# Performance work log

Measured on AMD Instinct MI355X. Metric: run time of the kernel, lower is better.

## Reference

```python
import jax, jax.numpy as jnp
import numpy as np

POINT_NB = 256
DILATION = 1
EPS = 1e-4  # pad mask value used by shiftFeat (0.0001)


def _shift(where, f, d):
    """Replicate-pad shift of f:[B,C,H,W]; returns shifted features and
    channel-averaged validity mask [B,1,H,W] (1 inside, EPS in pad region)."""
    B, C, H, W = f.shape
    m = jnp.ones((B, 1, H, W), dtype=f.dtype)
    if where == 'none':
        return f, m
    if where == 'left':
        fs = jnp.concatenate([f[..., d:], jnp.broadcast_to(f[..., -1:], (B, C, H, d))], axis=-1)
        m = m.at[..., -d:].set(EPS)
    elif where == 'right':
        fs = jnp.concatenate([jnp.broadcast_to(f[..., :1], (B, C, H, d)), f[..., :-d]], axis=-1)
        m = m.at[..., :d].set(EPS)
    elif where == 'top':
        fs = jnp.concatenate([f[:, :, d:, :], jnp.broadcast_to(f[:, :, -1:, :], (B, C, d, W))], axis=2)
        m = m.at[:, :, -d:, :].set(EPS)
    elif where == 'bot':
        fs = jnp.concatenate([jnp.broadcast_to(f[:, :, :1, :], (B, C, d, W)), f[:, :, :-d, :]], axis=2)
        m = m.at[:, :, :d, :].set(EPS)
    else:
        raise ValueError(where)
    return fs, m


def _cos_sim(f1, f2, m1, m2):
    # sim = sum(f1*f2*m1*m2, C) / (||m1*f1|| * ||m2*f2||); masks are [B,1,H,W], m>0
    num = (m1 * m2) * jnp.sum(f1 * f2, axis=1, keepdims=True)
    den = (m1 * jnp.sqrt(jnp.sum(f1 * f1, axis=1, keepdims=True))) * \
          (m2 * jnp.sqrt(jnp.sum(f2 * f2, axis=1, keepdims=True)))
    return num / den


def _total_sim(features, d):
    f1, m1 = _shift('right', features, d)
    f2, m2 = _shift('left', features, d)
    horiz = _cos_sim(f1, f2, m1, m2)
    f1, m1 = _shift('top', features, d)
    f2, m2 = _shift('bot', features, d)
    verti = _cos_sim(f1, f2, m1, m2)
    return (horiz + verti) * 0.5  # [B,1,H,W]


def setup_inputs() -> dict:
    key = jax.random.key(0)
    features = jax.random.normal(key, (16, 256, 56, 56), dtype=jnp.float32)
    return {"features": features}


def reference(features):
    B, C, H, W = features.shape
    sim = _total_sim(features, DILATION)            # [B,1,H,W]
    flat = sim.reshape(B, H * W)                    # [B,HW]
    vals, idx = jax.lax.top_k(flat, POINT_NB)       # [B,K]
    ycoord = idx // W
    xcoord = idx % W
    # gather feature vectors at selected points: [B,C,HW] -> [B,K,C]
    feat_flat = features.reshape(B, C, H * W)
    point_feat = jnp.take_along_axis(feat_flat, idx[:, None, :], axis=2)
    point_feat = jnp.transpose(point_feat, (0, 2, 1))
    return point_feat, vals, ycoord, xcoord
```

## Files before the change

kernel.cpp:

```cpp
#include <hip/hip_runtime.h>

#define NB 16
#define NC 256
#define NH 56
#define NW 56
#define NHW (NH * NW)
#define NK 256
#define CAP 1024

#define BR 8
#define RS 10
#define CS 8
#define CQ 64
#define NCHUNK (CQ / CS)
#define CHUNK16 (CS * RS * NW / 4)
#define NBAND (NH / BR)
#define P1_BLOCKS (NB * NBAND * 4)
#define NQ (BR * (NW / 4))
#define MAPS (NB * NHW)

#define GPX 112
#define GNT (NHW / GPX)
#define GCC 64
#define GCH16 (GCC * GPX * 4 / 16)

__device__ inline unsigned int flip_f32(float f) {
    unsigned int u = __float_as_uint(f);
    return (u & 0x80000000u) ? ~u : (u | 0x80000000u);
}
__device__ inline float unflip_f32(unsigned int u) {
    u = (u & 0x80000000u) ? (u ^ 0x80000000u) : ~u;
    return __uint_as_float(u);
}

__global__ void __launch_bounds__(256)
pass1_kernel(const float* __restrict__ f, float* __restrict__ maps) {
    __shared__ __align__(16) float buf[2][CS * RS * NW];
    __shared__ float redbuf[NQ][2][12];

    int bid = blockIdx.x;
    int sb = (bid & 7) * (P1_BLOCKS / 8) + (bid >> 3);
    int b = sb / 28;
    int rem0 = sb - b * 28;
    int band = rem0 >> 2;
    int chq = rem0 & 3;
    int y0 = band * BR;
    int tid = threadIdx.x;
    const float* fb = f + (size_t)b * NC * NHW + (size_t)chq * CQ * NHW;

    auto stage = [&](int ci, float* dst) {
        int c0 = ci * CS;
#pragma unroll
        for (int i = 0; i < 5; ++i) {
            int k = tid + 256 * i;
            if (k < CHUNK16) {
                int ch = k / (RS * 14);
                int rem = k - ch * (RS * 14);
                int rl = rem / 14;
                int xk = rem - rl * 14;
                int rg = y0 - 1 + rl;
                rg = rg < 0 ? 0 : (rg > NH - 1 ? NH - 1 : rg);
                const float* src = fb + (size_t)(c0 + ch) * NHW + rg * NW + xk * 4;
                __builtin_amdgcn_global_load_lds(
                    (const __attribute__((address_space(1))) void*)src,
                    (__attribute__((address_space(3))) void*)(dst + k * 4),
                    16, 0, 0);
            }
        }
    };

    int chg = tid / NQ;
    int quad = tid - chg * NQ;
    int r = quad / 14, qx = quad - r * 14, x0 = qx * 4;
    int xl = x0 ? x0 - 1 : 0;
    int xr = (x0 + 4 < NW) ? x0 + 4 : NW - 1;

    float n0 = 0.f, n1 = 0.f, n2 = 0.f, n3 = 0.f;
    float h0 = 0.f, h1 = 0.f, h2 = 0.f, h3 = 0.f;
    float w0 = 0.f, w1 = 0.f, w2 = 0.f, w3 = 0.f;

    stage(0, buf[0]);
    __syncthreads();
    for (int ci = 0; ci < NCHUNK; ++ci) {
        if (ci + 1 < NCHUNK) stage(ci + 1, buf[(ci + 1) & 1]);
        if (tid < 2 * NQ) {
            const float* sbf = buf[ci & 1];
#pragma unroll
            for (int c = 0; c < 4; ++c) {
                const float* Bm = sbf + (chg * 4 + c) * (RS * NW) + (r + 1) * NW;
                float4 v = *(const float4*)(Bm + x0);
                float  l = Bm[xl];
                float  rr = Bm[xr];
                float4 u = *(const float4*)(Bm + NW + x0);
                float4 d = *(const float4*)(Bm - NW + x0);
                n0 += v.x * v.x; n1 += v.y * v.y; n2 += v.z * v.z; n3 += v.w * v.w;
                h0 += l * v.y;   h1 += v.x * v.z; h2 += v.y * v.w; h3 += v.z * rr;
                w0 += u.x * d.x; w1 += u.y * d.y; w2 += u.z * d.z; w3 += u.w * d.w;
            }
        }
        __syncthreads();
    }

    if (tid < 2 * NQ) {
        float* rb = redbuf[quad][chg];
        rb[0] = n0; rb[1] = n1; rb[2]  = n2; rb[3]  = n3;
        rb[4] = h0; rb[5] = h1; rb[6]  = h2; rb[7]  = h3;
        rb[8] = w0; rb[9] = w1; rb[10] = w2; rb[11] = w3;
    }
    __syncthreads();

    float* mbase = maps + (size_t)chq * 3 * MAPS;
    for (int oi = tid; oi < NQ * 12; oi += 256) {
        int q = oi / 12, comp = oi - q * 12;
        float acc = redbuf[q][0][comp] + redbuf[q][1][comp];
        int r2 = q / 14, qx2 = q - r2 * 14;
        int j = comp & 3;
        float* m = mbase + (size_t)(comp >> 2) * MAPS;
        m[((size_t)b * NH + y0 + r2) * NW + qx2 * 4 + j] = acc;
    }
}

__global__ void __launch_bounds__(256)
sim_kernel(const float* __restrict__ maps, unsigned int* __restrict__ sv) {
    int pix = blockIdx.x * 256 + threadIdx.x;
    if (pix >= NB * NHW) return;
    int b = pix / NHW, i = pix - b * NHW;

    int y = i / NW, x = i - y * NW;
    int xl = (x > 0) ? x - 1 : 0;
    int xr = (x < NW - 1) ? x + 1 : NW - 1;
    int yu = (y < NH - 1) ? y + 1 : NH - 1;
    int yd = (y > 0) ? y - 1 : 0;
    int il = y * NW + xl, ir = y * NW + xr;
    int iu = yu * NW + x, id = yd * NW + x;

    float nl = 0.f, nr = 0.f, nu = 0.f, nd = 0.f, h = 0.f, v = 0.f;
#pragma unroll
    for (int q = 0; q < 4; ++q) {
        const float* nq = maps + (size_t)(q * 3 + 0) * MAPS + (size_t)b * NHW;
        const float* hq = maps + (size_t)(q * 3 + 1) * MAPS + (size_t)b * NHW;
        const float* vq = maps + (size_t)(q * 3 + 2) * MAPS + (size_t)b * NHW;
        nl += nq[il]; nr += nq[ir]; nu += nq[iu]; nd += nq[id];
        h  += hq[i];  v  += vq[i];
    }
    float s = 0.5f * (h / (sqrtf(nl) * sqrtf(nr)) + v / (sqrtf(nu) * sqrtf(nd)));
    sv[pix] = flip_f32(s);
}

__global__ void __launch_bounds__(1024)
topk_kernel(const unsigned int* __restrict__ sv, int* __restrict__ idx_out,
            float* __restrict__ vals_out, float* __restrict__ y_out,
            float* __restrict__ x_out) {
    __shared__ unsigned int svals[NHW];
    __shared__ unsigned int hist[4096];
    __shared__ unsigned int wtot[16];
    __shared__ unsigned long long cand[CAP];
    __shared__ unsigned int sh_prefix, sh_mask;
    __shared__ int sh_above, sh_setS, sh_done, sh_cnt;

    const int b = blockIdx.x;
    const int tid = threadIdx.x;
    const int lane = tid & 63;
    const int wv = tid >> 6;
    const unsigned int* svb = sv + (size_t)b * NHW;

    for (int i = tid; i < NHW; i += 1024) svals[i] = svb[i];
    if (tid == 0) { sh_prefix = 0u; sh_mask = 0u; sh_above = 0; sh_done = 0; }

    const int shifts[3] = {20, 8, 0};
    const unsigned int wmasks[3] = {0xFFFu, 0xFFFu, 0xFFu};
    for (int st = 0; st < 3; ++st) {
        __syncthreads();
        int kneed = NK - sh_above;
        if (sh_done) break;
        for (int i = tid; i < 4096; i += 1024) hist[i] = 0u;
        __syncthreads();
        unsigned int pfx = sh_prefix, msk = sh_mask;
        int shift = shifts[st];
        unsigned int wmask = wmasks[st];
        for (int i = tid; i < NHW; i += 1024) {
            unsigned int v = svals[i];
            if ((v & msk) == pfx) atomicAdd(&hist[(v >> shift) & wmask], 1u);
        }
        __syncthreads();
        unsigned int b0 = hist[4 * tid], b1 = hist[4 * tid + 1];
        unsigned int b2 = hist[4 * tid + 2], b3 = hist[4 * tid + 3];
        unsigned int lsum = b0 + b1 + b2 + b3;
        unsigned int s = lsum;
#pragma unroll
        for (int d = 1; d < 64; d <<= 1) {
            unsigned int t2 = __shfl_down(s, d);
            s += (lane + d < 64) ? t2 : 0u;
        }
        if (lane == 0) wtot[wv] = s;
        __syncthreads();
        unsigned int wabove = 0;
        for (int w = wv + 1; w < 16; ++w) wabove += wtot[w];
        unsigned int thr_above = wabove + (s - lsum);
        unsigned int suf3 = thr_above + b3;
        unsigned int suf2 = suf3 + b2;
        unsigned int suf1 = suf2 + b1;
        unsigned int suf0 = suf1 + b0;
        if (suf0 >= (unsigned int)kneed && thr_above < (unsigned int)kneed) {
            int c; unsigned int above, hc;
            if (suf3 >= (unsigned int)kneed)      { c = 4 * tid + 3; above = thr_above; hc = b3; }
            else if (suf2 >= (unsigned int)kneed) { c = 4 * tid + 2; above = suf3;      hc = b2; }
            else if (suf1 >= (unsigned int)kneed) { c = 4 * tid + 1; above = suf2;      hc = b1; }
            else                                  { c = 4 * tid + 0; above = suf1;      hc = b0; }
            sh_above += (int)above;
            sh_setS = (int)hc;
            sh_prefix = pfx | ((unsigned int)c << shift);
            sh_mask = msk | (wmask << shift);
            if (sh_above + sh_setS <= CAP || st == 2) sh_done = 1;
        }
    }
    __syncthreads();

    if (tid == 0) sh_cnt = 0;
    __syncthreads();
    unsigned int T = sh_prefix;
    for (int i = tid; i < NHW; i += 1024) {
        unsigned int v = svals[i];
        bool keep = (v >= T);
        unsigned long long m = __ballot(keep);
        int basep = 0;
        if (lane == 0) basep = atomicAdd(&sh_cnt, __popcll(m));
        basep = __shfl(basep, 0);
        if (keep) {
            int pos = basep + __popcll(m & ((1ull << lane) - 1ull));
            if (pos < CAP)
                cand[pos] = ((unsigned long long)v << 32) |
                            (unsigned long long)(0xFFFFFFFFu - (unsigned int)i);
        }
    }
    __syncthreads();
    int nc = sh_cnt; if (nc > CAP) nc = CAP;

    if (tid < nc) {
        unsigned long long my = cand[tid];
        int rank = 0;
        for (int i = 0; i < nc; ++i) rank += (cand[i] > my);
        if (rank < NK) {
            unsigned int lo = (unsigned int)(my & 0xFFFFFFFFull);
            int idx = (int)(0xFFFFFFFFu - lo);
            float val = unflip_f32((unsigned int)(my >> 32));
            int o = b * NK + rank;
            idx_out[o] = idx;
            vals_out[o] = val;
            y_out[o] = (float)(idx / NW);
            x_out[o] = (float)(idx % NW);
        }
    }
}

__global__ void __launch_bounds__(256)
gather_kernel(const float* __restrict__ f, const int* __restrict__ idx,
              float* __restrict__ out) {
    __shared__ __align__(16) float buf[2][GCC * GPX];

    int bid = blockIdx.x;
    int b = bid / GNT;
    int p0 = (bid - b * GNT) * GPX;
    int tid = threadIdx.x;
    const float* fB = f + (size_t)b * NC * NHW;

    int p = idx[b * NK + tid];
    int o = p - p0;
    bool mine = (o >= 0) && (o < GPX);
    float* outp = out + ((size_t)b * NK + tid) * NC;

    auto stage = [&](int ci, float* dst) {
        int c0 = ci * GCC;
#pragma unroll
        for (int i = 0; i < 7; ++i) {
            int k = tid + 256 * i;
            int ch = k / (GPX / 4);
            int xk = k - ch * (GPX / 4);
            const float* src = fB + (size_t)(c0 + ch) * NHW + p0 + xk * 4;
            __builtin_amdgcn_global_load_lds(
                (const __attribute__((address_space(1))) void*)src,
                (__attribute__((address_space(3))) void*)(dst + k * 4),
                16, 0, 0);
        }
    };

    stage(0, buf[0]);
    __syncthreads();
    for (int ci = 0; ci < 4; ++ci) {
        if (ci + 1 < 4) stage(ci + 1, buf[(ci + 1) & 1]);
        if (mine) {
            const float* sbf = buf[ci & 1];
            float* op = outp + ci * GCC;
#pragma unroll
            for (int g = 0; g < GCC / 4; ++g) {
                float4 w;
                w.x = sbf[(4 * g + 0) * GPX + o];
                w.y = sbf[(4 * g + 1) * GPX + o];
                w.z = sbf[(4 * g + 2) * GPX + o];
                w.w = sbf[(4 * g + 3) * GPX + o];
                *(float4*)(op + 4 * g) = w;
            }
        }
        __syncthreads();
    }
}

extern "C" void kernel_launch(void* const* d_in, const int* in_sizes, int n_in,
                              void* d_out, int out_size, void* d_ws, size_t ws_size,
                              hipStream_t stream) {
    const float* f = (const float*)d_in[0];

    float* out_feat = (float*)d_out;
    float* out_vals = out_feat + (size_t)NB * NK * NC;
    float* out_y    = out_vals + (size_t)NB * NK;
    float* out_x    = out_y    + (size_t)NB * NK;

    float* maps = (float*)d_ws;
    unsigned int* sv = (unsigned int*)(maps + 12 * (size_t)MAPS);
    int* idx = (int*)(sv + MAPS);

    pass1_kernel<<<P1_BLOCKS, 256, 0, stream>>>(f, maps);
    sim_kernel<<<(NB * NHW + 255) / 256, 256, 0, stream>>>(maps, sv);
    topk_kernel<<<NB, 1024, 0, stream>>>(sv, idx, out_vals, out_y, out_x);
    gather_kernel<<<NB * GNT, 256, 0, stream>>>(f, idx, out_feat);
}
```

Before: 38.84 us.

## Fuse similarity computation into top-k and restructure gather to single-stage tiles

Removes the separate sim kernel. The top-k kernel now sums the norm maps into shared memory and computes the cosine similarity per pixel itself, which saves one launch and a global round trip of the sim values. The gather kernel now uses 56-pixel tiles loading all 256 channels at once instead of double-buffered 64-channel chunks, and applies an XCD-style block swizzle. The catch is that top-k runs on only 16 blocks, so the fused similarity work there has little parallelism. The gather also issues twice as many blocks, each loading a larger tile.

```diff
diff --git a/kernel.cpp b/kernel.cpp
--- a/kernel.cpp
+++ b/kernel.cpp
@@ -19,10 +19,10 @@
 #define NQ (BR * (NW / 4))
 #define MAPS (NB * NHW)
 
-#define GPX 112
+#define GPX 56
 #define GNT (NHW / GPX)
-#define GCC 64
-#define GCH16 (GCC * GPX * 4 / 16)
+#define G_BLOCKS (NB * GNT)
+#define GCH16 (NC * GPX / 4)
 
 __device__ inline unsigned int flip_f32(float f) {
     unsigned int u = __float_as_uint(f);
@@ -120,37 +120,11 @@
     }
 }
 
-__global__ void __launch_bounds__(256)
-sim_kernel(const float* __restrict__ maps, unsigned int* __restrict__ sv) {
-    int pix = blockIdx.x * 256 + threadIdx.x;
-    if (pix >= NB * NHW) return;
-    int b = pix / NHW, i = pix - b * NHW;
-
-    int y = i / NW, x = i - y * NW;
-    int xl = (x > 0) ? x - 1 : 0;
-    int xr = (x < NW - 1) ? x + 1 : NW - 1;
-    int yu = (y < NH - 1) ? y + 1 : NH - 1;
-    int yd = (y > 0) ? y - 1 : 0;
-    int il = y * NW + xl, ir = y * NW + xr;
-    int iu = yu * NW + x, id = yd * NW + x;
-
-    float nl = 0.f, nr = 0.f, nu = 0.f, nd = 0.f, h = 0.f, v = 0.f;
-#pragma unroll
-    for (int q = 0; q < 4; ++q) {
-        const float* nq = maps + (size_t)(q * 3 + 0) * MAPS + (size_t)b * NHW;
-        const float* hq = maps + (size_t)(q * 3 + 1) * MAPS + (size_t)b * NHW;
-        const float* vq = maps + (size_t)(q * 3 + 2) * MAPS + (size_t)b * NHW;
-        nl += nq[il]; nr += nq[ir]; nu += nq[iu]; nd += nq[id];
-        h  += hq[i];  v  += vq[i];
-    }
-    float s = 0.5f * (h / (sqrtf(nl) * sqrtf(nr)) + v / (sqrtf(nu) * sqrtf(nd)));
-    sv[pix] = flip_f32(s);
-}
-
 __global__ void __launch_bounds__(1024)
-topk_kernel(const unsigned int* __restrict__ sv, int* __restrict__ idx_out,
+topk_kernel(const float* __restrict__ maps, int* __restrict__ idx_out,
             float* __restrict__ vals_out, float* __restrict__ y_out,
             float* __restrict__ x_out) {
+    __shared__ float nsh[NHW];
     __shared__ unsigned int svals[NHW];
     __shared__ unsigned int hist[4096];
     __shared__ unsigned int wtot[16];
@@ -162,10 +136,35 @@
     const int tid = threadIdx.x;
     const int lane = tid & 63;
     const int wv = tid >> 6;
-    const unsigned int* svb = sv + (size_t)b * NHW;
-
-    for (int i = tid; i < NHW; i += 1024) svals[i] = svb[i];
+
+    for (int i = tid; i < NHW; i += 1024) {
+        float n = 0.f;
+#pragma unroll
+        for (int q = 0; q < 4; ++q)
+            n += maps[(size_t)(q * 3 + 0) * MAPS + (size_t)b * NHW + i];
+        nsh[i] = n;
+    }
     if (tid == 0) { sh_prefix = 0u; sh_mask = 0u; sh_above = 0; sh_done = 0; }
+    __syncthreads();
+
+    for (int i = tid; i < NHW; i += 1024) {
+        int y = i / NW, x = i - y * NW;
+        int xl = (x > 0) ? x - 1 : 0;
+        int xr = (x < NW - 1) ? x + 1 : NW - 1;
+        int yu = (y < NH - 1) ? y + 1 : NH - 1;
+        int yd = (y > 0) ? y - 1 : 0;
+        int il = y * NW + xl, ir = y * NW + xr;
+        int iu = yu * NW + x, id = yd * NW + x;
+        float h = 0.f, v = 0.f;
+#pragma unroll
+        for (int q = 0; q < 4; ++q) {
+            h += maps[(size_t)(q * 3 + 1) * MAPS + (size_t)b * NHW + i];
+            v += maps[(size_t)(q * 3 + 2) * MAPS + (size_t)b * NHW + i];
+        }
+        float s = 0.5f * (h / (sqrtf(nsh[il]) * sqrtf(nsh[ir])) +
+                          v / (sqrtf(nsh[iu]) * sqrtf(nsh[id])));
+        svals[i] = flip_f32(s);
+    }
 
     const int shifts[3] = {20, 8, 0};
     const unsigned int wmasks[3] = {0xFFFu, 0xFFFu, 0xFFu};
@@ -256,52 +255,43 @@
 __global__ void __launch_bounds__(256)
 gather_kernel(const float* __restrict__ f, const int* __restrict__ idx,
               float* __restrict__ out) {
-    __shared__ __align__(16) float buf[2][GCC * GPX];
+    __shared__ __align__(16) float buf[NC * GPX];
 
     int bid = blockIdx.x;
-    int b = bid / GNT;
-    int p0 = (bid - b * GNT) * GPX;
+    int sb = (bid & 7) * (G_BLOCKS / 8) + (bid >> 3);
+    int b = sb / GNT;
+    int p0 = (sb - b * GNT) * GPX;
     int tid = threadIdx.x;
     const float* fB = f + (size_t)b * NC * NHW;
 
     int p = idx[b * NK + tid];
     int o = p - p0;
     bool mine = (o >= 0) && (o < GPX);
-    float* outp = out + ((size_t)b * NK + tid) * NC;
-
-    auto stage = [&](int ci, float* dst) {
-        int c0 = ci * GCC;
-#pragma unroll
-        for (int i = 0; i < 7; ++i) {
-            int k = tid + 256 * i;
-            int ch = k / (GPX / 4);
-            int xk = k - ch * (GPX / 4);
-            const float* src = fB + (size_t)(c0 + ch) * NHW + p0 + xk * 4;
-            __builtin_amdgcn_global_load_lds(
-                (const __attribute__((address_space(1))) void*)src,
-                (__attribute__((address_space(3))) void*)(dst + k * 4),
-                16, 0, 0);
-        }
-    };
-
-    stage(0, buf[0]);
-    __syncthreads();
-    for (int ci = 0; ci < 4; ++ci) {
-        if (ci + 1 < 4) stage(ci + 1, buf[(ci + 1) & 1]);
-        if (mine) {
-            const float* sbf = buf[ci & 1];
-            float* op = outp + ci * GCC;
-#pragma unroll
-            for (int g = 0; g < GCC / 4; ++g) {
-                float4 w;
-                w.x = sbf[(4 * g + 0) * GPX + o];
-                w.y = sbf[(4 * g + 1) * GPX + o];
-                w.z = sbf[(4 * g + 2) * GPX + o];
-                w.w = sbf[(4 * g + 3) * GPX + o];
-                *(float4*)(op + 4 * g) = w;
-            }
-        }
-        __syncthreads();
+
+#pragma unroll
+    for (int i = 0; i < 14; ++i) {
+        int k = tid + 256 * i;
+        int ch = k / (GPX / 4);
+        int xk = k - ch * (GPX / 4);
+        const float* src = fB + (size_t)ch * NHW + p0 + xk * 4;
+        __builtin_amdgcn_global_load_lds(
+            (const __attribute__((address_space(1))) void*)src,
+            (__attribute__((address_space(3))) void*)(buf + k * 4),
+            16, 0, 0);
+    }
+    __syncthreads();
+
+    if (mine) {
+        float* op = out + ((size_t)b * NK + tid) * NC;
+#pragma unroll
+        for (int g = 0; g < NC / 4; ++g) {
+            float4 w;
+            w.x = buf[(4 * g + 0) * GPX + o];
+            w.y = buf[(4 * g + 1) * GPX + o];
+            w.z = buf[(4 * g + 2) * GPX + o];
+            w.w = buf[(4 * g + 3) * GPX + o];
+            *(float4*)(op + 4 * g) = w;
+        }
     }
 }
 
@@ -316,11 +306,9 @@
     float* out_x    = out_y    + (size_t)NB * NK;
 
     float* maps = (float*)d_ws;
-    unsigned int* sv = (unsigned int*)(maps + 12 * (size_t)MAPS);
-    int* idx = (int*)(sv + MAPS);
+    int* idx = (int*)(maps + 12 * (size_t)MAPS);
 
     pass1_kernel<<<P1_BLOCKS, 256, 0, stream>>>(f, maps);
-    sim_kernel<<<(NB * NHW + 255) / 256, 256, 0, stream>>>(maps, sv);
-    topk_kernel<<<NB, 1024, 0, stream>>>(sv, idx, out_vals, out_y, out_x);
-    gather_kernel<<<NB * GNT, 256, 0, stream>>>(f, idx, out_feat);
-}
+    topk_kernel<<<NB, 1024, 0, stream>>>(maps, idx, out_vals, out_y, out_x);
+    gather_kernel<<<G_BLOCKS, 256, 0, stream>>>(f, idx, out_feat);
+}
```

Result: slower. 40.78 us (+5.0%).
